# Optimization experiments

Measured on AMD Instinct MI355X. Metric: run time of the kernel, lower is better.

## Reference

```python
import jax, jax.numpy as jnp
import numpy as np

D_MODEL = 512
NUM_HEADS = 8
HEAD_DIM = D_MODEL // NUM_HEADS
NEG_INF = -1e9


def setup_inputs() -> dict:
    key = jax.random.key(0)
    ks = jax.random.split(key, 12)
    B, S = 4, 2048
    std = 1.0 / np.sqrt(D_MODEL)
    inp = {
        "query": jax.random.normal(ks[0], (B, S, D_MODEL), jnp.float32),
        "key": jax.random.normal(ks[1], (B, S, D_MODEL), jnp.float32),
        "value": jax.random.normal(ks[2], (B, S, D_MODEL), jnp.float32),
        "mask": jax.random.randint(ks[3], (B, 1, S, S), 0, 2, jnp.int32),
        "Wq": jax.random.normal(ks[4], (D_MODEL, D_MODEL), jnp.float32) * std,
        "bq": jnp.zeros((D_MODEL,), jnp.float32),
        "Wk": jax.random.normal(ks[5], (D_MODEL, D_MODEL), jnp.float32) * std,
        "bk": jnp.zeros((D_MODEL,), jnp.float32),
        "Wv": jax.random.normal(ks[6], (D_MODEL, D_MODEL), jnp.float32) * std,
        "bv": jnp.zeros((D_MODEL,), jnp.float32),
        "Wo": jax.random.normal(ks[7], (D_MODEL, D_MODEL), jnp.float32) * std,
        "bo": jnp.zeros((D_MODEL,), jnp.float32),
    }
    return inp


def _split_heads(x):
    B, S, _ = x.shape
    return x.reshape(B, S, NUM_HEADS, HEAD_DIM).transpose(0, 2, 1, 3)  # [B,H,S,Dh]


def reference(query, key, value, mask, Wq, bq, Wk, bk, Wv, bv, Wo, bo):
    B, S, _ = query.shape
    q = _split_heads(query @ Wq + bq)
    k = _split_heads(key @ Wk + bk)
    v = _split_heads(value @ Wv + bv)
    # scores: [B,H,S,S]
    scores = jnp.einsum("bhqd,bhkd->bhqk", q, k) / jnp.sqrt(jnp.float32(HEAD_DIM))
    scores = jnp.where(mask == 0, jnp.float32(NEG_INF), scores)
    attn = jax.nn.softmax(scores, axis=-1)  # dropout p=0 -> identity
    out = jnp.einsum("bhqk,bhkd->bhqd", attn, v)
    out = out.transpose(0, 2, 1, 3).reshape(B, S, D_MODEL)
    return out @ Wo + bo
```

## Files before the change

kernel.cpp:

```cpp
#include <hip/hip_runtime.h>
#include <hip/hip_bf16.h>

typedef unsigned short u16;
typedef __attribute__((ext_vector_type(4))) float f32x4;
typedef __attribute__((ext_vector_type(8))) short s16x8;
typedef __attribute__((ext_vector_type(4))) unsigned short u16x4;

__device__ __forceinline__ u16 f2bf(float f) {
    union { float f; unsigned u; } v; v.f = f;
    unsigned r = v.u + 0x7fffu + ((v.u >> 16) & 1u);
    return (u16)(r >> 16);
}
__device__ __forceinline__ u16 f2bfh(float f) {
    __hip_bfloat16 h = __float2bfloat16(f);
    return *reinterpret_cast<u16*>(&h);
}
__device__ __forceinline__ float fexp2(float x) {
#if __has_builtin(__builtin_amdgcn_exp2f)
    return __builtin_amdgcn_exp2f(x);
#else
    return exp2f(x);
#endif
}
__device__ __forceinline__ void gload16(const void* g, void* lds_uniform) {
    __builtin_amdgcn_global_load_lds(
        (const __attribute__((address_space(1))) void*)g,
        (__attribute__((address_space(3))) void*)lds_uniform, 16, 0, 0);
}
__device__ __forceinline__ f32x4 mfma16(s16x8 a, s16x8 b, f32x4 c) {
    return __builtin_amdgcn_mfma_f32_16x16x32_bf16(a, b, c, 0, 0, 0);
}

__global__ void prep(const float4* __restrict__ q, const float4* __restrict__ k,
                     const float4* __restrict__ v, u16x4* __restrict__ qkv,
                     const float* __restrict__ Wq, const float* __restrict__ Wk,
                     const float* __restrict__ Wv, const float* __restrict__ Wo,
                     u16* __restrict__ WqT, u16* __restrict__ WkT,
                     u16* __restrict__ WvT, u16* __restrict__ WoT,
                     const int* __restrict__ mask, unsigned* __restrict__ bits) {
    __shared__ float tile[32][33];
    const int bid = blockIdx.x, tid = threadIdx.x;
    if (bid < 12288) {
        int i = bid * 256 + tid;
        int sel = i >> 20, j = i & 0xFFFFF;
        const float4* in = (sel == 0) ? q : (sel == 1) ? k : v;
        float4 f = in[j];
        u16x4 o;
        o[0] = f2bf(f.x); o[1] = f2bf(f.y); o[2] = f2bf(f.z); o[3] = f2bf(f.w);
        qkv[i] = o;
    } else if (bid < 13312) {
        int idx = bid - 12288;
        int bz = idx >> 8, rem = idx & 255, by = rem >> 4, bx = rem & 15;
        const float* W; u16* T;
        switch (bz) {
            case 0: W = Wq; T = WqT; break;
            case 1: W = Wk; T = WkT; break;
            case 2: W = Wv; T = WvT; break;
            default: W = Wo; T = WoT; break;
        }
        const int tx = tid & 31, ty = tid >> 5;
        const int k0 = by * 32, n0 = bx * 32;
#pragma unroll
        for (int r = 0; r < 32; r += 8) tile[ty + r][tx] = W[(k0 + ty + r) * 512 + n0 + tx];
        __syncthreads();
#pragma unroll
        for (int r = 0; r < 32; r += 8) T[(n0 + ty + r) * 512 + k0 + tx] = f2bf(tile[tx][ty + r]);
    } else {
        int i = (bid - 13312) * 256 + tid;
        int m = mask[i];
        unsigned long long bal = __ballot(m != 0);
        if ((tid & 63) == 0) {
            uint2 w2; w2.x = (unsigned)bal; w2.y = (unsigned)(bal >> 32);
            *(uint2*)&bits[i >> 5] = w2;
        }
    }
}

template <int BM, int BIAS_ROW, int OUT_F32>
__global__ __launch_bounds__(256, 4) void gemm_bt(
    const u16* __restrict__ A, const u16* __restrict__ Bt0, const u16* __restrict__ Bt1,
    const float* __restrict__ bias0, const float* __restrict__ bias1,
    void* __restrict__ Cout, int M, int N, int K, int ysplit,
    float scale0, float scale1) {
    constexpr int MR = BM / 32;
    const u16* Bt = (blockIdx.y < (unsigned)ysplit) ? Bt0 : Bt1;
    const float* bias = (blockIdx.y < (unsigned)ysplit) ? bias0 : bias1;
    const float scale = (blockIdx.y < (unsigned)ysplit) ? scale0 : scale1;
    __shared__ u16 As[BM * 32];
    __shared__ u16 Bs[64 * 32];
    const int t = threadIdx.x, l = t & 63, w = t >> 6;
    const int lr = l & 15, lg = l >> 4;
    const int m0 = blockIdx.y * BM, n0 = blockIdx.x * 64;
    const int wr = w >> 1, wc = w & 1;
    f32x4 acc[MR][2] = {};
    const int ar = t >> 2, ac = (t & 3) * 8;

    for (int kk = 0; kk < K; kk += 32) {
        __syncthreads();
        gload16(A + (m0 + ar) * K + kk + ac, As + w * 512);
        if (BM == 128)
            gload16(A + (m0 + 64 + ar) * K + kk + ac, As + 2048 + w * 512);
        gload16(Bt + (n0 + ar) * K + kk + ac, Bs + w * 512);
        __syncthreads();
        s16x8 af[MR], bfr[2];
#pragma unroll
        for (int m = 0; m < MR; ++m)
            af[m] = *(const s16x8*)&As[(wr * (BM / 2) + m * 16 + lr) * 32 + lg * 8];
#pragma unroll
        for (int n = 0; n < 2; ++n)
            bfr[n] = *(const s16x8*)&Bs[(wc * 32 + n * 16 + lr) * 32 + lg * 8];
#pragma unroll
        for (int m = 0; m < MR; ++m)
#pragma unroll
            for (int n = 0; n < 2; ++n) acc[m][n] = mfma16(af[m], bfr[n], acc[m][n]);
    }

#pragma unroll
    for (int n = 0; n < 2; ++n) {
        const int cg = n0 + wc * 32 + n * 16 + lr;
        const float bcol = BIAS_ROW ? 0.f : bias[cg];
#pragma unroll
        for (int m = 0; m < MR; ++m) {
            const int rbase = m0 + wr * (BM / 2) + m * 16 + lg * 4;
#pragma unroll
            for (int j = 0; j < 4; ++j) {
                const int rg = rbase + j;
                float val = (acc[m][n][j] + (BIAS_ROW ? bias[rg] : bcol)) * scale;
                if (OUT_F32) ((float*)Cout)[(size_t)rg * N + cg] = val;
                else         ((u16*)Cout)[(size_t)rg * N + cg] = f2bf(val);
            }
        }
    }
}

__global__ __launch_bounds__(256, 4) void attn_fwd(
    const u16* __restrict__ Qp, const u16* __restrict__ Kp,
    const u16* __restrict__ Vt, const unsigned* __restrict__ mbits,
    u16* __restrict__ AO) {
    constexpr int S = 2048;
    const int qt = blockIdx.x, bh = blockIdx.y;
    const int b = bh >> 3, h = bh & 7;
    const int t = threadIdx.x, l = t & 63, w = t >> 6;
    const int lr = l & 15, lg = l >> 4;

    __shared__ u16 Ks[2][64 * 64];
    __shared__ u16 Vs[2][64 * 64];
    __shared__ u16 Ps[4][16 * 64];

    const int q0 = qt * 64 + w * 16;
    const int bS = b * S;

    s16x8 qf[2];
#pragma unroll
    for (int ks = 0; ks < 2; ++ks)
        qf[ks] = *(const s16x8*)&Qp[(bS + q0 + lr) * 512 + h * 64 + ks * 32 + lg * 8];

    f32x4 po[4] = {};
    float lrun[4] = {0.f, 0.f, 0.f, 0.f};

    const int kc0 = t, kc1 = 256 + t;
    const int krow0 = kc0 >> 3, kcol0 = ((kc0 & 7) ^ (krow0 & 7)) * 8;
    const int krow1 = kc1 >> 3, kcol1 = ((kc1 & 7) ^ (krow1 & 7)) * 8;

#define STAGE(nb, kt0)                                                              \
    do {                                                                            \
        gload16(&Kp[(bS + (kt0) + krow0) * 512 + h * 64 + kcol0], &Ks[nb][w * 512]);\
        gload16(&Kp[(bS + (kt0) + krow1) * 512 + h * 64 + kcol1], &Ks[nb][2048 + w * 512]);\
        gload16(&Vt[(h * 64 + krow0) * (4 * S) + bS + (kt0) + kcol0], &Vs[nb][w * 512]);\
        gload16(&Vt[(h * 64 + krow1) * (4 * S) + bS + (kt0) + kcol1], &Vs[nb][2048 + w * 512]);\
    } while (0)

    uint2 mw[4], mwn[4];
    STAGE(0, 0);
#pragma unroll
    for (int jj = 0; jj < 4; ++jj)
        mw[jj] = *(const uint2*)&mbits[(bS + q0 + lg * 4 + jj) * 64];
#pragma unroll
    for (int jj = 0; jj < 4; ++jj) mwn[jj] = mw[jj];

    for (int it = 0; it < 32; ++it) {
        const int cur = it & 1;
        __syncthreads();
        if (it + 1 < 32) {
            STAGE(cur ^ 1, (it + 1) * 64);
#pragma unroll
            for (int jj = 0; jj < 4; ++jj)
                mwn[jj] = *(const uint2*)&mbits[(bS + q0 + lg * 4 + jj) * 64 + ((it + 1) << 1)];
        }
        const u16* Kc = Ks[cur];
        const u16* Vc = Vs[cur];

        f32x4 sc[4];
#pragma unroll
        for (int nk = 0; nk < 4; ++nk) sc[nk] = f32x4{0.f, 0.f, 0.f, 0.f};
        __builtin_amdgcn_s_setprio(1);
#pragma unroll
        for (int nk = 0; nk < 4; ++nk) {
            const int ktc = nk * 16 + lr;
            const int sw = (ktc & 7) << 4;
            s16x8 k0 = *(const s16x8*)((const char*)Kc + ((ktc * 128 + lg * 16) ^ sw));
            s16x8 k1 = *(const s16x8*)((const char*)Kc + ((ktc * 128 + 64 + lg * 16) ^ sw));
            sc[nk] = mfma16(qf[0], k0, sc[nk]);
            sc[nk] = mfma16(qf[1], k1, sc[nk]);
        }
        __builtin_amdgcn_s_setprio(0);

#pragma unroll
        for (int nk = 0; nk < 4; ++nk) {
            const unsigned bp = ((nk & 1) << 4) + lr;
#pragma unroll
            for (int jj = 0; jj < 4; ++jj) {
                const unsigned word = (nk >> 1) ? mw[jj].y : mw[jj].x;
                const float s = ((word >> bp) & 1u) ? sc[nk][jj] : -1e9f;
                sc[nk][jj] = fexp2(s);
            }
        }
#pragma unroll
        for (int jj = 0; jj < 4; ++jj)
            lrun[jj] += (sc[0][jj] + sc[1][jj]) + (sc[2][jj] + sc[3][jj]);

#pragma unroll
        for (int nk = 0; nk < 4; ++nk) {
            const int ktc = nk * 16 + lr;
#pragma unroll
            for (int jj = 0; jj < 4; ++jj) {
                const int qloc = lg * 4 + jj;
                const int byte = (qloc * 128 + ktc * 2) ^ ((qloc & 7) << 4);
                *(u16*)((char*)&Ps[w][0] + byte) = f2bfh(sc[nk][jj]);
            }
        }

        s16x8 pa[2];
#pragma unroll
        for (int k2 = 0; k2 < 2; ++k2) {
            const int byte = (lr * 128 + k2 * 64 + lg * 16) ^ ((lr & 7) << 4);
            pa[k2] = *(const s16x8*)((const char*)&Ps[w][0] + byte);
        }

        __builtin_amdgcn_s_setprio(1);
#pragma unroll
        for (int dn = 0; dn < 4; ++dn) {
            const int d = dn * 16 + lr;
            const int sw = (d & 7) << 4;
            s16x8 v0 = *(const s16x8*)((const char*)Vc + ((d * 128 + lg * 16) ^ sw));
            s16x8 v1 = *(const s16x8*)((const char*)Vc + ((d * 128 + 64 + lg * 16) ^ sw));
            po[dn] = mfma16(pa[0], v0, po[dn]);
            po[dn] = mfma16(pa[1], v1, po[dn]);
        }
        __builtin_amdgcn_s_setprio(0);

#pragma unroll
        for (int jj = 0; jj < 4; ++jj) mw[jj] = mwn[jj];
    }
#undef STAGE

#pragma unroll
    for (int jj = 0; jj < 4; ++jj) {
        float s = lrun[jj];
        s += __shfl_xor(s, 1);
        s += __shfl_xor(s, 2);
        s += __shfl_xor(s, 4);
        s += __shfl_xor(s, 8);
        const float inv = 1.f / s;
        const int q = q0 + lg * 4 + jj;
#pragma unroll
        for (int dn = 0; dn < 4; ++dn)
            AO[(bS + q) * 512 + h * 64 + dn * 16 + lr] = f2bfh(po[dn][jj] * inv);
    }
}

extern "C" void kernel_launch(void* const* d_in, const int* in_sizes, int n_in,
                              void* d_out, int out_size, void* d_ws, size_t ws_size,
                              hipStream_t stream) {
    (void)in_sizes; (void)n_in; (void)out_size; (void)ws_size;
    const float* query = (const float*)d_in[0];
    const float* key   = (const float*)d_in[1];
    const float* value = (const float*)d_in[2];
    const int*   mask  = (const int*)d_in[3];
    const float* Wq = (const float*)d_in[4];
    const float* bq = (const float*)d_in[5];
    const float* Wk = (const float*)d_in[6];
    const float* bk = (const float*)d_in[7];
    const float* Wv = (const float*)d_in[8];
    const float* bv = (const float*)d_in[9];
    const float* Wo = (const float*)d_in[10];
    const float* bo = (const float*)d_in[11];

    char* ws = (char*)d_ws;
    const size_t MB = 1ull << 20;
    u16* qb  = (u16*)(ws);
    u16* vb  = (u16*)(ws + 16 * MB);
    u16* WqT = (u16*)(ws + 24 * MB);
    u16* WkT = (u16*)(ws + 24 * MB + 512 * 1024);
    u16* WvT = (u16*)(ws + 25 * MB);
    u16* WoT = (u16*)(ws + 25 * MB + 512 * 1024);
    unsigned* mb = (unsigned*)(ws + 26 * MB);
    u16* Qp = (u16*)(ws + 28 * MB);
    u16* Vt = (u16*)(ws + 44 * MB);
    u16* AO = (u16*)(ws + 52 * MB);

    prep<<<78848, 256, 0, stream>>>((const float4*)query, (const float4*)key,
                                    (const float4*)value, (u16x4*)qb,
                                    Wq, Wk, Wv, Wo, WqT, WkT, WvT, WoT, mask, mb);

    gemm_bt<128, 0, 0><<<dim3(8, 128), 256, 0, stream>>>(
        qb, WqT, WkT, bq, bk, Qp, 16384, 512, 512, 64, 0.18033688f, 1.0f);
    gemm_bt<64, 1, 0><<<dim3(128, 8), 256, 0, stream>>>(
        WvT, vb, vb, bv, bv, Vt, 512, 8192, 512, 999, 1.0f, 1.0f);

    attn_fwd<<<dim3(32, 32), 256, 0, stream>>>(Qp, Qp + 8192 * 512, Vt, mb, AO);

    gemm_bt<64, 0, 1><<<dim3(8, 128), 256, 0, stream>>>(
        AO, WoT, WoT, bo, bo, (float*)d_out, 8192, 512, 512, 999, 1.0f, 1.0f);
}
```

Measured before the change: 157.0 us.

## Rewrite attention with 32x32 MFMA, register-resident P via permlane swap

The attention kernel switches from 16x16x32 to 32x32x16 bf16 MFMA and computes S transposed (K as A operand), so each wave covers 32 query rows and a block covers 128 rows. The probability tile is packed to bf16 with cvt_pk and redistributed across lane halves with v_permlane32_swap, so it is fed directly as the B operand of the PV MFMA without the LDS round trip through Ps. This also halves the grid, doubles K/V reuse per staged tile, and simplifies the mask and row-sum handling to one uint2 per lane. In exchange, register pressure rises (launch bounds lowered to 2 blocks per SM) and fewer blocks are available to fill the GPU.

After: 150.7 us. 4.1% less time.

```diff
diff --git a/kernel.cpp b/kernel.cpp
--- a/kernel.cpp
+++ b/kernel.cpp
@@ -3,6 +3,7 @@
 
 typedef unsigned short u16;
 typedef __attribute__((ext_vector_type(4))) float f32x4;
+typedef __attribute__((ext_vector_type(16))) float f32x16;
 typedef __attribute__((ext_vector_type(8))) short s16x8;
 typedef __attribute__((ext_vector_type(4))) unsigned short u16x4;
 
@@ -29,6 +30,9 @@
 }
 __device__ __forceinline__ f32x4 mfma16(s16x8 a, s16x8 b, f32x4 c) {
     return __builtin_amdgcn_mfma_f32_16x16x32_bf16(a, b, c, 0, 0, 0);
+}
+__device__ __forceinline__ f32x16 mfma32(s16x8 a, s16x8 b, f32x16 c) {
+    return __builtin_amdgcn_mfma_f32_32x32x16_bf16(a, b, c, 0, 0, 0);
 }
 
 __global__ void prep(const float4* __restrict__ q, const float4* __restrict__ k,
@@ -133,7 +137,7 @@
     }
 }
 
-__global__ __launch_bounds__(256, 4) void attn_fwd(
+__global__ __launch_bounds__(256, 2) void attn_fwd(
     const u16* __restrict__ Qp, const u16* __restrict__ Kp,
     const u16* __restrict__ Vt, const unsigned* __restrict__ mbits,
     u16* __restrict__ AO) {
@@ -141,22 +145,24 @@
     const int qt = blockIdx.x, bh = blockIdx.y;
     const int b = bh >> 3, h = bh & 7;
     const int t = threadIdx.x, l = t & 63, w = t >> 6;
-    const int lr = l & 15, lg = l >> 4;
+    const int lq = l & 31, hi = l >> 5;
+    const int hi8 = hi * 8, hi4 = hi * 4;
 
     __shared__ u16 Ks[2][64 * 64];
     __shared__ u16 Vs[2][64 * 64];
-    __shared__ u16 Ps[4][16 * 64];
-
-    const int q0 = qt * 64 + w * 16;
+
+    const int q0w = qt * 128 + w * 32;
     const int bS = b * S;
 
-    s16x8 qf[2];
-#pragma unroll
-    for (int ks = 0; ks < 2; ++ks)
-        qf[ks] = *(const s16x8*)&Qp[(bS + q0 + lr) * 512 + h * 64 + ks * 32 + lg * 8];
-
-    f32x4 po[4] = {};
-    float lrun[4] = {0.f, 0.f, 0.f, 0.f};
+    s16x8 qf[4];
+#pragma unroll
+    for (int ds = 0; ds < 4; ++ds)
+        qf[ds] = *(const s16x8*)&Qp[(bS + q0w + lq) * 512 + h * 64 + ds * 16 + hi8];
+
+    f32x16 po[2];
+#pragma unroll
+    for (int r = 0; r < 16; ++r) { po[0][r] = 0.f; po[1][r] = 0.f; }
+    float lrun = 0.f;
 
     const int kc0 = t, kc1 = 256 + t;
     const int krow0 = kc0 >> 3, kcol0 = ((kc0 & 7) ^ (krow0 & 7)) * 8;
@@ -170,103 +176,95 @@
         gload16(&Vt[(h * 64 + krow1) * (4 * S) + bS + (kt0) + kcol1], &Vs[nb][2048 + w * 512]);\
     } while (0)
 
-    uint2 mw[4], mwn[4];
     STAGE(0, 0);
-#pragma unroll
-    for (int jj = 0; jj < 4; ++jj)
-        mw[jj] = *(const uint2*)&mbits[(bS + q0 + lg * 4 + jj) * 64];
-#pragma unroll
-    for (int jj = 0; jj < 4; ++jj) mwn[jj] = mw[jj];
+    uint2 mwv = *(const uint2*)&mbits[(bS + q0w + lq) * 64];
+    uint2 mwn = mwv;
 
     for (int it = 0; it < 32; ++it) {
         const int cur = it & 1;
         __syncthreads();
         if (it + 1 < 32) {
             STAGE(cur ^ 1, (it + 1) * 64);
-#pragma unroll
-            for (int jj = 0; jj < 4; ++jj)
-                mwn[jj] = *(const uint2*)&mbits[(bS + q0 + lg * 4 + jj) * 64 + ((it + 1) << 1)];
+            mwn = *(const uint2*)&mbits[(bS + q0w + lq) * 64 + ((it + 1) << 1)];
         }
         const u16* Kc = Ks[cur];
         const u16* Vc = Vs[cur];
 
-        f32x4 sc[4];
-#pragma unroll
-        for (int nk = 0; nk < 4; ++nk) sc[nk] = f32x4{0.f, 0.f, 0.f, 0.f};
+        s16x8 bq[4];
+#pragma unroll
+        for (int kt_t = 0; kt_t < 2; ++kt_t) {
+            f32x16 sc;
+#pragma unroll
+            for (int r = 0; r < 16; ++r) sc[r] = 0.f;
+            __builtin_amdgcn_s_setprio(1);
+#pragma unroll
+            for (int ds = 0; ds < 4; ++ds) {
+                const int row = kt_t * 32 + lq;
+                const int byte = (row * 128 + ds * 32 + hi * 16) ^ ((row & 7) << 4);
+                s16x8 ka = *(const s16x8*)((const char*)Kc + byte);
+                sc = mfma32(ka, qf[ds], sc);
+            }
+            __builtin_amdgcn_s_setprio(0);
+
+            const unsigned w32 = kt_t ? mwv.y : mwv.x;
+            float p[16];
+            float ps = 0.f;
+#pragma unroll
+            for (int r = 0; r < 16; ++r) {
+                const int shift = (r & 3) + 8 * (r >> 2);
+                const float s = ((w32 >> (shift + hi4)) & 1u) ? sc[r] : -1e9f;
+                p[r] = fexp2(s);
+                ps += p[r];
+            }
+            lrun += ps;
+
+            unsigned pk[8];
+#pragma unroll
+            for (int i = 0; i < 8; ++i) {
+                unsigned v;
+                asm("v_cvt_pk_bf16_f32 %0, %1, %2"
+                    : "=v"(v) : "v"(p[2 * i]), "v"(p[2 * i + 1]));
+                pk[i] = v;
+            }
+            asm("v_permlane32_swap_b32 %0, %1" : "+v"(pk[0]), "+v"(pk[2]));
+            asm("v_permlane32_swap_b32 %0, %1" : "+v"(pk[1]), "+v"(pk[3]));
+            asm("v_permlane32_swap_b32 %0, %1" : "+v"(pk[4]), "+v"(pk[6]));
+            asm("v_permlane32_swap_b32 %0, %1" : "+v"(pk[5]), "+v"(pk[7]));
+            union BQ { unsigned u[4]; s16x8 v; } b0, b1;
+            b0.u[0] = pk[0]; b0.u[1] = pk[1]; b0.u[2] = pk[2]; b0.u[3] = pk[3];
+            b1.u[0] = pk[4]; b1.u[1] = pk[5]; b1.u[2] = pk[6]; b1.u[3] = pk[7];
+            bq[kt_t * 2]     = b0.v;
+            bq[kt_t * 2 + 1] = b1.v;
+        }
+
         __builtin_amdgcn_s_setprio(1);
 #pragma unroll
-        for (int nk = 0; nk < 4; ++nk) {
-            const int ktc = nk * 16 + lr;
-            const int sw = (ktc & 7) << 4;
-            s16x8 k0 = *(const s16x8*)((const char*)Kc + ((ktc * 128 + lg * 16) ^ sw));
-            s16x8 k1 = *(const s16x8*)((const char*)Kc + ((ktc * 128 + 64 + lg * 16) ^ sw));
-            sc[nk] = mfma16(qf[0], k0, sc[nk]);
-            sc[nk] = mfma16(qf[1], k1, sc[nk]);
-        }
+        for (int dt = 0; dt < 2; ++dt)
+#pragma unroll
+            for (int ks = 0; ks < 4; ++ks) {
+                const int row = dt * 32 + lq;
+                const int byte = (row * 128 + ks * 32 + hi * 16) ^ ((row & 7) << 4);
+                s16x8 va = *(const s16x8*)((const char*)Vc + byte);
+                po[dt] = mfma32(va, bq[ks], po[dt]);
+            }
         __builtin_amdgcn_s_setprio(0);
 
-#pragma unroll
-        for (int nk = 0; nk < 4; ++nk) {
-            const unsigned bp = ((nk & 1) << 4) + lr;
-#pragma unroll
-            for (int jj = 0; jj < 4; ++jj) {
-                const unsigned word = (nk >> 1) ? mw[jj].y : mw[jj].x;
-                const float s = ((word >> bp) & 1u) ? sc[nk][jj] : -1e9f;
-                sc[nk][jj] = fexp2(s);
-            }
-        }
-#pragma unroll
-        for (int jj = 0; jj < 4; ++jj)
-            lrun[jj] += (sc[0][jj] + sc[1][jj]) + (sc[2][jj] + sc[3][jj]);
-
-#pragma unroll
-        for (int nk = 0; nk < 4; ++nk) {
-            const int ktc = nk * 16 + lr;
-#pragma unroll
-            for (int jj = 0; jj < 4; ++jj) {
-                const int qloc = lg * 4 + jj;
-                const int byte = (qloc * 128 + ktc * 2) ^ ((qloc & 7) << 4);
-                *(u16*)((char*)&Ps[w][0] + byte) = f2bfh(sc[nk][jj]);
-            }
-        }
-
-        s16x8 pa[2];
-#pragma unroll
-        for (int k2 = 0; k2 < 2; ++k2) {
-            const int byte = (lr * 128 + k2 * 64 + lg * 16) ^ ((lr & 7) << 4);
-            pa[k2] = *(const s16x8*)((const char*)&Ps[w][0] + byte);
-        }
-
-        __builtin_amdgcn_s_setprio(1);
-#pragma unroll
-        for (int dn = 0; dn < 4; ++dn) {
-            const int d = dn * 16 + lr;
-            const int sw = (d & 7) << 4;
-            s16x8 v0 = *(const s16x8*)((const char*)Vc + ((d * 128 + lg * 16) ^ sw));
-            s16x8 v1 = *(const s16x8*)((const char*)Vc + ((d * 128 + 64 + lg * 16) ^ sw));
-            po[dn] = mfma16(pa[0], v0, po[dn]);
-            po[dn] = mfma16(pa[1], v1, po[dn]);
-        }
-        __builtin_amdgcn_s_setprio(0);
-
-#pragma unroll
-        for (int jj = 0; jj < 4; ++jj) mw[jj] = mwn[jj];
+        mwv = mwn;
     }
 #undef STAGE
 
-#pragma unroll
-    for (int jj = 0; jj < 4; ++jj) {
-        float s = lrun[jj];
-        s += __shfl_xor(s, 1);
-        s += __shfl_xor(s, 2);
-        s += __shfl_xor(s, 4);
-        s += __shfl_xor(s, 8);
-        const float inv = 1.f / s;
-        const int q = q0 + lg * 4 + jj;
-#pragma unroll
-        for (int dn = 0; dn < 4; ++dn)
-            AO[(bS + q) * 512 + h * 64 + dn * 16 + lr] = f2bfh(po[dn][jj] * inv);
-    }
+    lrun += __shfl_xor(lrun, 32);
+    const float inv = 1.f / lrun;
+    const int orow = (bS + q0w + lq) * 512 + h * 64;
+#pragma unroll
+    for (int dt = 0; dt < 2; ++dt)
+#pragma unroll
+        for (int r = 0; r < 16; r += 2) {
+            const int d = dt * 32 + (r & 3) + 8 * (r >> 2) + hi4;
+            const unsigned lo = f2bfh(po[dt][r] * inv);
+            const unsigned hh = f2bfh(po[dt][r + 1] * inv);
+            *(unsigned*)&AO[orow + d] = lo | (hh << 16);
+        }
 }
 
 extern "C" void kernel_launch(void* const* d_in, const int* in_sizes, int n_in,
@@ -308,7 +306,7 @@
     gemm_bt<64, 1, 0><<<dim3(128, 8), 256, 0, stream>>>(
         WvT, vb, vb, bv, bv, Vt, 512, 8192, 512, 999, 1.0f, 1.0f);
 
-    attn_fwd<<<dim3(32, 32), 256, 0, stream>>>(Qp, Qp + 8192 * 512, Vt, mb, AO);
+    attn_fwd<<<dim3(16, 32), 256, 0, stream>>>(Qp, Qp + 8192 * 512, Vt, mb, AO);
 
     gemm_bt<64, 0, 1><<<dim3(8, 128), 256, 0, stream>>>(
         AO, WoT, WoT, bo, bo, (float*)d_out, 8192, 512, 512, 999, 1.0f, 1.0f);
```
